# Kernel optimization log

Measured on AMD Instinct MI355X. Metric: run time of the kernel, lower is better.

Reference implementation:

```python
import jax, jax.numpy as jnp
import numpy as np

K = 20
EPS = 1e-5
SLOPE = 0.2


def _knn_idx(x, k):
    # x: [B, C, N] -> idx [B, N, k] of nearest neighbors by squared L2
    sq = jnp.sum(x * x, axis=1)                      # [B, N]
    inner = jnp.einsum('bcn,bcm->bnm', x, x)         # [B, N, N]
    neg_dist = 2.0 * inner - sq[:, :, None] - sq[:, None, :]
    return jax.lax.top_k(neg_dist, k)[1]             # [B, N, k]


def _edge_block(x, W, gamma, beta, k):
    # x: [B, C, N]; W: [O, 2C]; returns [B, O, N]
    idx = _knn_idx(x, k)
    xt = jnp.transpose(x, (0, 2, 1))                 # [B, N, C]
    nb = jax.vmap(lambda t, i: t[i])(xt, idx)        # [B, N, k, C] gather
    ctr = xt[:, :, None, :]
    edge = jnp.concatenate(
        [nb - ctr, jnp.broadcast_to(ctr, nb.shape)], axis=-1)  # [B, N, k, 2C]
    y = jnp.einsum('bnkc,oc->bonk', edge, W)         # 1x1 conv
    # BatchNorm2d (training mode: batch stats over B,N,k per channel)
    m = jnp.mean(y, axis=(0, 2, 3), keepdims=True)
    v = jnp.var(y, axis=(0, 2, 3), keepdims=True)
    y = (y - m) * jax.lax.rsqrt(v + EPS)
    y = y * gamma[None, :, None, None] + beta[None, :, None, None]
    y = jnp.where(y >= 0, y, SLOPE * y)              # LeakyReLU(0.2)
    return jnp.max(y, axis=-1)                       # max over k neighbors


def setup_inputs() -> dict:
    key = jax.random.key(0)
    ks = jax.random.split(key, 8)
    B, N = 8, 2048
    x = jax.random.normal(ks[0], (B, N, 3), dtype=jnp.float32)
    W1 = jax.random.normal(ks[1], (64, 6), dtype=jnp.float32) * 0.2
    W2 = jax.random.normal(ks[2], (128, 128), dtype=jnp.float32) * 0.08
    W3 = jax.random.normal(ks[3], (256, 256), dtype=jnp.float32) * 0.06
    g1, b1 = jnp.ones((64,), jnp.float32), jnp.zeros((64,), jnp.float32)
    g2, b2 = jnp.ones((128,), jnp.float32), jnp.zeros((128,), jnp.float32)
    g3, b3 = jnp.ones((256,), jnp.float32), jnp.zeros((256,), jnp.float32)
    L1 = jax.random.normal(ks[4], (1024, 448), dtype=jnp.float32) * 0.04
    L2 = jax.random.normal(ks[5], (2500, 1024), dtype=jnp.float32) * 0.03
    return {"x": x, "W1": W1, "g1": g1, "b1": b1, "W2": W2, "g2": g2,
            "b2": b2, "W3": W3, "g3": g3, "b3": b3, "L1": L1, "L2": L2}


def reference(x, W1, g1, b1, W2, g2, b2, W3, g3, b3, L1, L2):
    xT = jnp.transpose(x, (0, 2, 1))                 # [B, 3, N]
    x1 = _edge_block(xT, W1, g1, b1, K)              # [B, 64, N]
    x2 = _edge_block(x1, W2, g2, b2, K)              # [B, 128, N]
    x3 = _edge_block(x2, W3, g3, b3, K)              # [B, 256, N]
    feat = jnp.concatenate([x1, x2, x3], axis=1)     # [B, 448, N]
    pooled = jnp.max(feat, axis=-1)                  # adaptive_max_pool1d(1)
    h = pooled @ L1.T
    h = jnp.where(h >= 0, h, SLOPE * h)              # LeakyReLU(0.2)
    # dropout is identity in eval mode
    return h @ L2.T                                  # [B, 2500]
```

## Files before the change

### kernel.cpp

```cpp
#include <hip/hip_runtime.h>
#include <hip/hip_bf16.h>
#include <float.h>

#define K_NN 20
#define EPS 1e-5f
#define SLOPE 0.2f
constexpr int Bsz = 8;
constexpr int Npts = 2048;
constexpr int NQ = 8;
constexpr int BN = Bsz * Npts;

typedef __attribute__((ext_vector_type(8))) short short8v;
typedef __attribute__((ext_vector_type(4))) float f32x4;

__device__ __forceinline__ float dot4(float4 a, float4 b) {
  return a.x*b.x + a.y*b.y + a.z*b.z + a.w*b.w;
}
__device__ __forceinline__ unsigned encf(float f) {
  unsigned u = __float_as_uint(f);
  return (u & 0x80000000u) ? ~u : (u | 0x80000000u);
}
__device__ __forceinline__ float decf(unsigned e) {
  unsigned u = (e & 0x80000000u) ? (e & 0x7fffffffu) : ~e;
  return __uint_as_float(u);
}
__device__ __forceinline__ unsigned short f2bf(float x) {
  unsigned u = __float_as_uint(x);
  unsigned r = (u + 0x7fffu + ((u >> 16) & 1u)) >> 16;
  return (unsigned short)r;
}
__device__ __forceinline__ float bf2f(unsigned short h) {
  return __uint_as_float((unsigned)h << 16);
}
__device__ __forceinline__ f32x4 mfma16(short8v a, short8v b, f32x4 c) {
  return __builtin_amdgcn_mfma_f32_16x16x32_bf16(a, b, c, 0, 0, 0);
}

template<int C>
__global__ __launch_bounds__(256) void sq_kernel(const float* __restrict__ xt,
                                                 float* __restrict__ sq) {
  int p = blockIdx.x * 256 + threadIdx.x;
  if (p >= BN) return;
  const float* r = xt + (size_t)p * C;
  float s = 0.f;
  if constexpr (C % 4 == 0) {
    for (int c4 = 0; c4 < C / 4; ++c4) { float4 v = *(const float4*)(r + c4 * 4); s += dot4(v, v); }
  } else {
    #pragma unroll
    for (int c = 0; c < C; ++c) { float v = r[c]; s += v * v; }
  }
  sq[p] = s;
}

template<int C, int MT>
__global__ __launch_bounds__(256) void knn_part(const float* __restrict__ xt,
    const float* __restrict__ sq, float* __restrict__ pval, int* __restrict__ pidx) {
  constexpr int MQ = Npts / NQ;
  __shared__ __align__(16) float chk[MT][C];
  __shared__ float csq[MT];
  const int t = threadIdx.x, w = t >> 6, l = t & 63;
  const int rowblk = blockIdx.x / NQ;
  const int q = blockIdx.x - rowblk * NQ;
  const int p0 = rowblk * 256;
  const int b = p0 / Npts;
  const int myrow = p0 + w * 64 + l;

  float cr[C];
  #pragma unroll
  for (int c = 0; c < C; ++c) cr[c] = xt[(size_t)myrow * C + c];
  const float sqn = sq[myrow];

  float vals[K_NN]; int ids[K_NN];
  #pragma unroll
  for (int i = 0; i < K_NN; ++i) { vals[i] = -FLT_MAX; ids[i] = 0; }

  const int mbase = q * MQ;
  for (int m0 = mbase; m0 < mbase + MQ; m0 += MT) {
    __syncthreads();
    const float* s2 = xt + ((size_t)b * Npts + m0) * C;
    for (int e = t; e < MT * C; e += 256) chk[e / C][e - (e / C) * C] = s2[e];
    for (int e = t; e < MT; e += 256) csq[e] = sq[b * Npts + m0 + e];
    __syncthreads();
    for (int j = 0; j < MT; ++j) {
      float dt = 0.f;
      #pragma unroll
      for (int c = 0; c < C; ++c) dt += cr[c] * chk[j][c];
      float nd = 2.f * dt - sqn - csq[j];
      if (nd > vals[K_NN - 1]) {
        vals[K_NN - 1] = nd; ids[K_NN - 1] = m0 + j;
        #pragma unroll
        for (int i = K_NN - 1; i >= 1; --i) {
          if (vals[i] > vals[i - 1]) {
            float tv = vals[i]; vals[i] = vals[i-1]; vals[i-1] = tv;
            int ti = ids[i]; ids[i] = ids[i-1]; ids[i-1] = ti;
          }
        }
      }
    }
  }
  size_t base = ((size_t)q * BN + myrow) * K_NN;
  #pragma unroll
  for (int i = 0; i < K_NN; ++i) { pval[base + i] = vals[i]; pidx[base + i] = ids[i]; }
}

__global__ __launch_bounds__(256) void knn_merge(const float* __restrict__ pval,
    const int* __restrict__ pidx, int* __restrict__ idxout) {
  int p = blockIdx.x * 256 + threadIdx.x;
  if (p >= BN) return;
  float vals[K_NN]; int ids[K_NN];
  size_t base = (size_t)p * K_NN;
  #pragma unroll
  for (int i = 0; i < K_NN; ++i) { vals[i] = pval[base + i]; ids[i] = pidx[base + i]; }
  for (int q = 1; q < NQ; ++q) {
    size_t b2 = ((size_t)q * BN + p) * K_NN;
    #pragma unroll
    for (int i = 0; i < K_NN; ++i) {
      float v = pval[b2 + i];
      if (v <= vals[K_NN - 1]) break;
      int m = pidx[b2 + i];
      vals[K_NN - 1] = v; ids[K_NN - 1] = m;
      #pragma unroll
      for (int r = K_NN - 1; r >= 1; --r) {
        if (vals[r] > vals[r - 1]) {
          float tv = vals[r]; vals[r] = vals[r-1]; vals[r-1] = tv;
          int ti = ids[r]; ids[r] = ids[r-1]; ids[r-1] = ti;
        }
      }
    }
  }
  int* op = idxout + (size_t)p * K_NN;
  #pragma unroll
  for (int i = 0; i < K_NN; ++i) op[i] = ids[i];
}

template<int C>
__global__ __launch_bounds__(256, 1) void knn_fused(
    const unsigned short* __restrict__ xh, const unsigned short* __restrict__ xl,
    const float* __restrict__ sq, int* __restrict__ idxout) {
  constexpr int KS = C / 32;
  __shared__ __align__(16) char smem[40960];
  float (*dist)[66] = (float(*)[66])smem;
  float (*lv)[K_NN] = (float(*)[K_NN])smem;
  int   (*li)[K_NN] = (int(*)[K_NN])(smem + 256 * K_NN * 4);
  const int b = blockIdx.x >> 5, nt = blockIdx.x & 31;
  const int n0 = nt * 64;
  const int t = threadIdx.x, l = t & 63, wv = t >> 6, l15 = l & 15, grp = l >> 4;
  const unsigned short* xbh = xh + (size_t)b * Npts * C;
  const unsigned short* xbl = xl + (size_t)b * Npts * C;
  const float* sqb = sq + b * Npts;

  short8v ah[4 * KS], al[4 * KS];
  #pragma unroll
  for (int rt = 0; rt < 4; ++rt)
    #pragma unroll
    for (int ks = 0; ks < KS; ++ks) {
      const size_t a = (size_t)(n0 + rt * 16 + l15) * C + ks * 32 + grp * 8;
      ah[rt * KS + ks] = *(const short8v*)(xbh + a);
      al[rt * KS + ks] = *(const short8v*)(xbl + a);
    }

  const int srow = t >> 2, ss = t & 3;
  const float sqn = sqb[n0 + srow];
  float vals[K_NN]; int ids[K_NN];
  #pragma unroll
  for (int i = 0; i < K_NN; ++i) { vals[i] = -FLT_MAX; ids[i] = 0; }

  for (int mt = 0; mt < 32; ++mt) {
    const int m0 = mt * 64;
    const int brow = m0 + wv * 16 + l15;
    f32x4 acc[4];
    #pragma unroll
    for (int rt = 0; rt < 4; ++rt) acc[rt] = (f32x4){0.f, 0.f, 0.f, 0.f};
    #pragma unroll
    for (int ks = 0; ks < KS; ++ks) {
      const size_t boff = (size_t)brow * C + ks * 32 + grp * 8;
      const short8v bh = *(const short8v*)(xbh + boff);
      const short8v bl = *(const short8v*)(xbl + boff);
      #pragma unroll
      for (int rt = 0; rt < 4; ++rt) {
        acc[rt] = mfma16(ah[rt * KS + ks], bh, acc[rt]);
        acc[rt] = mfma16(al[rt * KS + ks], bh, acc[rt]);
        acc[rt] = mfma16(ah[rt * KS + ks], bl, acc[rt]);
      }
    }
    __syncthreads();
    #pragma unroll
    for (int rt = 0; rt < 4; ++rt)
      #pragma unroll
      for (int r = 0; r < 4; ++r)
        dist[rt * 16 + grp * 4 + r][wv * 16 + l15] = 2.f * acc[rt][r];
    __syncthreads();
    for (int j = 0; j < 16; ++j) {
      const int gcol = m0 + ss * 16 + j;
      float v = dist[srow][ss * 16 + j] - sqn - sqb[gcol];
      if (gcol == n0 + srow) v = 0.f;
      if (v > vals[K_NN - 1]) {
        vals[K_NN - 1] = v; ids[K_NN - 1] = gcol;
        #pragma unroll
        for (int r = K_NN - 1; r >= 1; --r) {
          if (vals[r] > vals[r - 1]) {
            float tv = vals[r]; vals[r] = vals[r-1]; vals[r-1] = tv;
            int ti = ids[r]; ids[r] = ids[r-1]; ids[r-1] = ti;
          }
        }
      }
    }
  }
  __syncthreads();
  #pragma unroll
  for (int i = 0; i < K_NN; ++i) { lv[t][i] = vals[i]; li[t][i] = ids[i]; }
  __syncthreads();
  if (t < 64) {
    float mv[K_NN]; int mi[K_NN];
    #pragma unroll
    for (int i = 0; i < K_NN; ++i) { mv[i] = lv[t * 4][i]; mi[i] = li[t * 4][i]; }
    for (int s2 = 1; s2 < 4; ++s2) {
      #pragma unroll
      for (int i = 0; i < K_NN; ++i) {
        const float v = lv[t * 4 + s2][i];
        if (v <= mv[K_NN - 1]) break;
        const int m = li[t * 4 + s2][i];
        mv[K_NN - 1] = v; mi[K_NN - 1] = m;
        #pragma unroll
        for (int r = K_NN - 1; r >= 1; --r) {
          if (mv[r] > mv[r - 1]) {
            float tv = mv[r]; mv[r] = mv[r-1]; mv[r-1] = tv;
            int ti = mi[r]; mi[r] = mi[r-1]; mi[r-1] = ti;
          }
        }
      }
    }
    int* op = idxout + ((size_t)(b * Npts + n0 + t)) * K_NN;
    #pragma unroll
    for (int i = 0; i < K_NN; ++i) op[i] = mi[i];
  }
}

template<int C, int O>
__global__ __launch_bounds__(256) void prep_w(const float* __restrict__ W,
    unsigned short* __restrict__ wh, unsigned short* __restrict__ wl) {
  int i = blockIdx.x * 256 + threadIdx.x;
  if (i >= 2 * O * C) return;
  int j = i / C, c = i - j * C;
  float v = (j < O) ? W[(size_t)j * 2 * C + c]
                    : (W[(size_t)(j - O) * 2 * C + C + c] - W[(size_t)(j - O) * 2 * C + c]);
  unsigned short h = f2bf(v);
  wh[i] = h; wl[i] = f2bf(v - bf2f(h));
}

template<int C, int N2>
__global__ __launch_bounds__(256) void zgemm(
    const unsigned short* __restrict__ xh, const unsigned short* __restrict__ xl,
    const unsigned short* __restrict__ wh, const unsigned short* __restrict__ wl,
    float* __restrict__ Z, int r0) {
  constexpr int KS = C / 32;
  constexpr int CB = N2 / 64;
  const int nb = blockIdx.x / CB, cb = blockIdx.x - nb * CB;
  const int ln0 = nb * 64;
  const int t = threadIdx.x, l = t & 63, wv = t >> 6, l15 = l & 15, grp = l >> 4;
  const int col = cb * 64 + wv * 16 + l15;
  f32x4 acc[4];
  #pragma unroll
  for (int rt = 0; rt < 4; ++rt) acc[rt] = (f32x4){0.f, 0.f, 0.f, 0.f};
  #pragma unroll
  for (int ks = 0; ks < KS; ++ks) {
    const int krd = ks * 32 + grp * 8;
    const short8v bh = *(const short8v*)(wh + (size_t)col * C + krd);
    const short8v bl = *(const short8v*)(wl + (size_t)col * C + krd);
    #pragma unroll
    for (int rt = 0; rt < 4; ++rt) {
      const size_t arow = (size_t)(r0 + ln0 + rt * 16 + l15) * C + krd;
      const short8v a_h = *(const short8v*)(xh + arow);
      const short8v a_l = *(const short8v*)(xl + arow);
      acc[rt] = mfma16(a_h, bh, acc[rt]);
      acc[rt] = mfma16(a_l, bh, acc[rt]);
      acc[rt] = mfma16(a_h, bl, acc[rt]);
    }
  }
  #pragma unroll
  for (int rt = 0; rt < 4; ++rt)
    #pragma unroll
    for (int r = 0; r < 4; ++r)
      Z[(size_t)(ln0 + rt * 16 + grp * 4 + r) * N2 + col] = acc[rt][r];
}

template<int O, int NPP>
__global__ __launch_bounds__(256) void nbr_reduce(
    const float* __restrict__ Z, const int* __restrict__ idx,
    float* __restrict__ mx, float* __restrict__ mn,
    float* __restrict__ psum, float* __restrict__ psq, int r0) {
  constexpr int PPB = 256 / O;
  constexpr int O2 = 2 * O;
  const int t = threadIdx.x;
  const int o = t % O;
  const int sub = t / O;
  float ls = 0.f, lq = 0.f;
  for (int it = 0; it < NPP / PPB; ++it) {
    const int p = r0 + blockIdx.x * NPP + it * PPB + sub;
    const int bbase = (p >> 11) << 11;
    const int* ip = idx + (size_t)p * K_NN;
    const float base = Z[(size_t)(p - r0) * O2 + O + o];
    float vmx = -FLT_MAX, vmn = FLT_MAX;
    #pragma unroll
    for (int k = 0; k < K_NN; ++k) {
      const int nbrow = bbase + ip[k] - r0;
      const float y = Z[(size_t)nbrow * O2 + o] + base;
      ls += y; lq = fmaf(y, y, lq);
      vmx = fmaxf(vmx, y); vmn = fminf(vmn, y);
    }
    mx[(size_t)p * O + o] = vmx;
    mn[(size_t)p * O + o] = vmn;
  }
  if constexpr (PPB > 1) {
    __shared__ float s1[256], s2[256];
    s1[t] = ls; s2[t] = lq;
    __syncthreads();
    if (sub == 0) {
      psum[(size_t)blockIdx.x * O + o] = ls + s1[t + O];
      psq [(size_t)blockIdx.x * O + o] = lq + s2[t + O];
    }
  } else {
    psum[(size_t)blockIdx.x * O + o] = ls;
    psq [(size_t)blockIdx.x * O + o] = lq;
  }
}

template<int C, int O, int G, int NPG, int CPT>
__global__ __launch_bounds__(256) void edge_kernel(const float* __restrict__ xt,
    const int* __restrict__ idx, const float* __restrict__ W,
    float* __restrict__ mx, float* __restrict__ mn,
    float* __restrict__ psum, float* __restrict__ psq) {
  constexpr int WP = O / (64 * CPT);
  constexpr int TPB = 64 * WP * NPG;
  constexpr int PPG = G / NPG;
  static_assert(TPB == 256, "block must be 256 threads");
  __shared__ __align__(16) float pts[G][K_NN + 1][C];
  __shared__ int ids[G][K_NN + 1];
  __shared__ float shps[NPG][O];
  __shared__ float shpq[NPG][O];
  const int t = threadIdx.x;
  const int p0 = blockIdx.x * G;
  const int b = p0 / Npts;

  for (int e = t; e < G * (K_NN + 1); e += TPB) {
    int g = e / (K_NN + 1), j = e - g * (K_NN + 1);
    ids[g][j] = (j == 0) ? (p0 + g) : (b * Npts + idx[(size_t)(p0 + g) * K_NN + (j - 1)]);
  }
  __syncthreads();
  for (int e = t; e < G * (K_NN + 1) * C; e += TPB) {
    int g = e / ((K_NN + 1) * C), rem = e - g * ((K_NN + 1) * C);
    int j = rem / C, c = rem - j * C;
    pts[g][j][c] = xt[(size_t)ids[g][j] * C + c];
  }
  __syncthreads();

  const int w = t >> 6, l = t & 63;
  const int pg = w / WP, wp = w - pg * WP;
  const int o0 = wp * 64 + l;
  float ls0 = 0.f, lq0 = 0.f;

  for (int it = 0; it < PPG; ++it) {
    const int g = pg * PPG + it;
    float yk0[K_NN];
    float u0 = 0.f, v0 = 0.f;
    #pragma unroll
    for (int k = 0; k < K_NN; ++k) yk0[k] = 0.f;
    const float* W0 = W + (size_t)o0 * (2 * C);
    #pragma unroll
    for (int c = 0; c < C; ++c) {
      const float wl = W0[c], whv = W0[C + c], ccv = pts[g][0][c];
      u0 += wl * ccv; v0 += whv * ccv;
      #pragma unroll
      for (int k = 0; k < K_NN; ++k) yk0[k] += wl * pts[g][k + 1][c];
    }
    const int n = p0 + g - b * Npts;
    const size_t obase = ((size_t)b * Npts + n) * O;
    const float base = v0 - u0;
    float vmx = -FLT_MAX, vmn = FLT_MAX;
    #pragma unroll
    for (int k = 0; k < K_NN; ++k) {
      float y = yk0[k] + base;
      ls0 += y; lq0 += y * y;
      vmx = fmaxf(vmx, y); vmn = fminf(vmn, y);
    }
    mx[obase + o0] = vmx; mn[obase + o0] = vmn;
  }

  shps[pg][o0] = ls0; shpq[pg][o0] = lq0;
  __syncthreads();
  if (t < O) {
    float s = 0.f, qq = 0.f;
    #pragma unroll
    for (int i = 0; i < NPG; ++i) { s += shps[i][t]; qq += shpq[i][t]; }
    psum[(size_t)blockIdx.x * O + t] = s;
    psq [(size_t)blockIdx.x * O + t] = qq;
  }
}

template<int O, int NBLK>
__global__ __launch_bounds__(256) void stats_part(const float* __restrict__ psum,
    const float* __restrict__ psq, double* __restrict__ pp, double* __restrict__ pq) {
  constexpr int NS = 16;
  constexpr int SL = NBLK / NS;
  const int l = threadIdx.x & 63, w = threadIdx.x >> 6;
  const int os = blockIdx.x % (O / 64), sl = blockIdx.x / (O / 64);
  const int o = os * 64 + l;
  double s = 0.0, ss = 0.0;
  for (int i = sl * SL + w; i < (sl + 1) * SL; i += 4) {
    s  += (double)psum[(size_t)i * O + o];
    ss += (double)psq [(size_t)i * O + o];
  }
  __shared__ double sh[2][4][64];
  sh[0][w][l] = s; sh[1][w][l] = ss;
  __syncthreads();
  if (w == 0) {
    s  = sh[0][0][l] + sh[0][1][l] + sh[0][2][l] + sh[0][3][l];
    ss = sh[1][0][l] + sh[1][1][l] + sh[1][2][l] + sh[1][3][l];
    pp[(size_t)sl * O + o] = s;
    pq[(size_t)sl * O + o] = ss;
  }
}

template<int O>
__global__ __launch_bounds__(64) void stats_final(const double* __restrict__ pp,
    const double* __restrict__ pq,
    const float* __restrict__ gamma, const float* __restrict__ beta,
    float* __restrict__ scale, float* __restrict__ bias) {
  const int o = blockIdx.x * 64 + threadIdx.x;
  double s = 0.0, ss = 0.0;
  #pragma unroll
  for (int sl = 0; sl < 16; ++sl) { s += pp[(size_t)sl * O + o]; ss += pq[(size_t)sl * O + o]; }
  double cnt = (double)Bsz * Npts * K_NN;
  double m = s / cnt;
  double var = ss / cnt - m * m;
  float g = gamma[o];
  float sc = g * rsqrtf((float)var + EPS);
  scale[o] = sc;
  bias[o] = beta[o] - (float)m * sc;
}

__global__ __launch_bounds__(256) void reset_pool(unsigned* __restrict__ pooled) {
  int i = blockIdx.x * 256 + threadIdx.x;
  if (i < Bsz * 448) pooled[i] = 0u;
}

template<int O, int COFF, bool WNC>
__global__ __launch_bounds__(256) void apply_kernel(const float* __restrict__ mx,
    const float* __restrict__ mn, const float* __restrict__ scale,
    const float* __restrict__ bias, float* __restrict__ xnc,
    unsigned short* __restrict__ xh, unsigned short* __restrict__ xl,
    unsigned* __restrict__ pooled) {
  constexpr int OT = O / 64;
  constexpr int NCH = Npts / 256;
  const int bid = blockIdx.x;
  const int nchunk = bid % NCH;
  const int ot = (bid / NCH) % OT;
  const int b = bid / (NCH * OT);
  const int l = threadIdx.x & 63, w = threadIdx.x >> 6;
  const int o = ot * 64 + l;
  const float sc = scale[o], bs = bias[o];
  const bool pos = (sc >= 0.f);
  float vmax = -FLT_MAX;
  const int n0 = nchunk * 256;
  for (int i = 0; i < 64; ++i) {
    int n = n0 + w + i * 4;
    size_t ix = ((size_t)b * Npts + n) * O + o;
    float raw = pos ? mx[ix] : mn[ix];
    float y = raw * sc + bs;
    y = (y >= 0.f) ? y : SLOPE * y;
    if constexpr (WNC) {
      xnc[ix] = y;
      unsigned short h = f2bf(y);
      xh[ix] = h;
      xl[ix] = f2bf(y - bf2f(h));
    }
    vmax = fmaxf(vmax, y);
  }
  __shared__ float sh[4][64];
  sh[w][l] = vmax;
  __syncthreads();
  if (w == 0) {
    float m = fmaxf(fmaxf(sh[0][l], sh[1][l]), fmaxf(sh[2][l], sh[3][l]));
    atomicMax(pooled + b * 448 + COFF + o, encf(m));
  }
}

template<int CIN, bool LRELU, bool DECODE>
__global__ __launch_bounds__(64) void fc_kernel(const void* __restrict__ inv,
    const float* __restrict__ Wt, float* __restrict__ out, int JO) {
  int j = blockIdx.x;
  const float* wr = Wt + (size_t)j * CIN;
  float acc[Bsz];
  #pragma unroll
  for (int b = 0; b < Bsz; ++b) acc[b] = 0.f;
  for (int c = threadIdx.x; c < CIN; c += 64) {
    float wv = wr[c];
    #pragma unroll
    for (int b = 0; b < Bsz; ++b) {
      float x;
      if constexpr (DECODE) x = decf(((const unsigned*)inv)[b * CIN + c]);
      else                  x = ((const float*)inv)[b * CIN + c];
      acc[b] += x * wv;
    }
  }
  #pragma unroll
  for (int b = 0; b < Bsz; ++b) {
    float v = acc[b];
    #pragma unroll
    for (int w = 32; w > 0; w >>= 1) v += __shfl_down(v, w);
    if (threadIdx.x == 0) {
      if (LRELU) v = (v >= 0.f) ? v : SLOPE * v;
      out[b * JO + j] = v;
    }
  }
}

extern "C" void kernel_launch(void* const* d_in, const int* in_sizes, int n_in,
                              void* d_out, int out_size, void* d_ws, size_t ws_size,
                              hipStream_t stream) {
  const float* x   = (const float*)d_in[0];
  const float* W1  = (const float*)d_in[1];
  const float* g1  = (const float*)d_in[2];
  const float* b1  = (const float*)d_in[3];
  const float* W2  = (const float*)d_in[4];
  const float* g2  = (const float*)d_in[5];
  const float* b2  = (const float*)d_in[6];
  const float* W3  = (const float*)d_in[7];
  const float* g3  = (const float*)d_in[8];
  const float* b3  = (const float*)d_in[9];
  const float* L1  = (const float*)d_in[10];
  const float* L2  = (const float*)d_in[11];
  float* out = (float*)d_out;

  float* ws = (float*)d_ws;
  size_t off = 0;
  float* sq    = ws + off; off += BN;
  int*   idxb  = (int*)(ws + off); off += (size_t)BN * K_NN;
  float* mx    = ws + off; off += (size_t)BN * 256;
  float* mn    = ws + off; off += (size_t)BN * 256;
  float* Z     = ws + off; off += (size_t)BN * 256;
  float* psum  = ws + off; off += (size_t)2048 * 256;
  float* psq   = ws + off; off += (size_t)2048 * 256;
  off = (off + 1) & ~(size_t)1;
  double* pp   = (double*)(ws + off); off += 16 * 256 * 2;
  double* pq   = (double*)(ws + off); off += 16 * 256 * 2;
  float* scale = ws + off; off += 256;
  float* bias  = ws + off; off += 256;
  float* x1nc  = ws + off; off += (size_t)BN * 64;
  float* x2nc  = ws + off; off += (size_t)BN * 128;
  unsigned short* xh1 = (unsigned short*)(ws + off); off += (size_t)BN * 64 / 2;
  unsigned short* xl1 = (unsigned short*)(ws + off); off += (size_t)BN * 64 / 2;
  unsigned short* xh2 = (unsigned short*)(ws + off); off += (size_t)BN * 128 / 2;
  unsigned short* xl2 = (unsigned short*)(ws + off); off += (size_t)BN * 128 / 2;
  unsigned* pooled = (unsigned*)(ws + off); off += Bsz * 448;
  float* h     = ws + off; off += Bsz * 1024;
  unsigned short* wch2 = (unsigned short*)(ws + off); off += 256 * 64 / 2;
  unsigned short* wcl2 = (unsigned short*)(ws + off); off += 256 * 64 / 2;
  unsigned short* wch3 = (unsigned short*)(ws + off); off += 512 * 128 / 2;
  unsigned short* wcl3 = (unsigned short*)(ws + off); off += 512 * 128 / 2;
  float* pval = mx;
  int*   pidx = (int*)mn;

  reset_pool<<<14, 256, 0, stream>>>(pooled);
  prep_w<64, 128><<<(2 * 128 * 64 + 255) / 256, 256, 0, stream>>>(W2, wch2, wcl2);
  prep_w<128, 256><<<(2 * 256 * 128 + 255) / 256, 256, 0, stream>>>(W3, wch3, wcl3);

  sq_kernel<3><<<64, 256, 0, stream>>>(x, sq);
  knn_part<3, 64><<<(BN / 256) * NQ, 256, 0, stream>>>(x, sq, pval, pidx);
  knn_merge<<<64, 256, 0, stream>>>(pval, pidx, idxb);
  edge_kernel<3, 64, 16, 4, 1><<<BN / 16, 256, 0, stream>>>(x, idxb, W1, mx, mn, psum, psq);
  stats_part<64, 1024><<<16, 256, 0, stream>>>(psum, psq, pp, pq);
  stats_final<64><<<1, 64, 0, stream>>>(pp, pq, g1, b1, scale, bias);
  apply_kernel<64, 0, true><<<64, 256, 0, stream>>>(mx, mn, scale, bias, x1nc, xh1, xl1, pooled);

  sq_kernel<64><<<64, 256, 0, stream>>>(x1nc, sq);
  knn_fused<64><<<Bsz * 32, 256, 0, stream>>>(xh1, xl1, sq, idxb);
  zgemm<64, 256><<<(BN / 64) * 4, 256, 0, stream>>>(xh1, xl1, wch2, wcl2, Z, 0);
  nbr_reduce<128, 16><<<BN / 16, 256, 0, stream>>>(Z, idxb, mx, mn, psum, psq, 0);
  stats_part<128, 1024><<<32, 256, 0, stream>>>(psum, psq, pp, pq);
  stats_final<128><<<2, 64, 0, stream>>>(pp, pq, g2, b2, scale, bias);
  apply_kernel<128, 64, true><<<128, 256, 0, stream>>>(mx, mn, scale, bias, x2nc, xh2, xl2, pooled);

  sq_kernel<128><<<64, 256, 0, stream>>>(x2nc, sq);
  knn_fused<128><<<Bsz * 32, 256, 0, stream>>>(xh2, xl2, sq, idxb);
  for (int pass = 0; pass < 2; ++pass) {
    const int r0 = pass * (BN / 2);
    zgemm<128, 512><<<(BN / 2 / 64) * 8, 256, 0, stream>>>(xh2, xl2, wch3, wcl3, Z, r0);
    nbr_reduce<256, 8><<<BN / 2 / 8, 256, 0, stream>>>(Z, idxb, mx, mn,
        psum + (size_t)pass * 1024 * 256, psq + (size_t)pass * 1024 * 256, r0);
  }
  stats_part<256, 2048><<<64, 256, 0, stream>>>(psum, psq, pp, pq);
  stats_final<256><<<4, 64, 0, stream>>>(pp, pq, g3, b3, scale, bias);
  apply_kernel<256, 192, false><<<256, 256, 0, stream>>>(mx, mn, scale, bias, nullptr, nullptr, nullptr, pooled);

  fc_kernel<448, true, true><<<1024, 64, 0, stream>>>(pooled, L1, h, 1024);
  fc_kernel<1024, false, false><<<2500, 64, 0, stream>>>(h, L2, out, 2500);
}
```

Before: 1.248 ms.

## Restructure knn_fused into single-wave blocks with in-register top-k and shuffle merge

The fused kNN kernel now runs one 64-lane wave per block, each handling 16 query points. Each wave keeps the query fragments in registers and streams all candidate tiles through MFMA. Distances are consumed straight from the accumulator registers, so the LDS staging, the __syncthreads barriers and the LDS-based merge are gone; the four per-lane partial top-k lists are merged with shuffles. This raises block count from 256 to 1024 to fill more CUs. In exchange, the candidate loads are re-read per wave with less reuse across query rows, and the per-lane insertion sorts get more divergent work.

```diff
diff --git a/kernel.cpp b/kernel.cpp
--- a/kernel.cpp
+++ b/kernel.cpp
@@ -134,68 +134,86 @@
 }
 
 template<int C>
-__global__ __launch_bounds__(256, 1) void knn_fused(
+__global__ __launch_bounds__(64) void knn_fused(
     const unsigned short* __restrict__ xh, const unsigned short* __restrict__ xl,
     const float* __restrict__ sq, int* __restrict__ idxout) {
   constexpr int KS = C / 32;
-  __shared__ __align__(16) char smem[40960];
-  float (*dist)[66] = (float(*)[66])smem;
-  float (*lv)[K_NN] = (float(*)[K_NN])smem;
-  int   (*li)[K_NN] = (int(*)[K_NN])(smem + 256 * K_NN * 4);
-  const int b = blockIdx.x >> 5, nt = blockIdx.x & 31;
-  const int n0 = nt * 64;
-  const int t = threadIdx.x, l = t & 63, wv = t >> 6, l15 = l & 15, grp = l >> 4;
+  const int b = blockIdx.x >> 7, qt = blockIdx.x & 127;
+  const int q0 = qt * 16;
+  const int l = threadIdx.x, l15 = l & 15, grp = l >> 4;
   const unsigned short* xbh = xh + (size_t)b * Npts * C;
   const unsigned short* xbl = xl + (size_t)b * Npts * C;
   const float* sqb = sq + b * Npts;
-
-  short8v ah[4 * KS], al[4 * KS];
-  #pragma unroll
-  for (int rt = 0; rt < 4; ++rt)
+  const int qi = q0 + l15;
+
+  short8v bh[KS], bl[KS];
+  #pragma unroll
+  for (int ks = 0; ks < KS; ++ks) {
+    const size_t a = (size_t)qi * C + ks * 32 + grp * 8;
+    bh[ks] = *(const short8v*)(xbh + a);
+    bl[ks] = *(const short8v*)(xbl + a);
+  }
+  const float sqn = sqb[qi];
+
+  float vals[K_NN]; int ids[K_NN];
+  #pragma unroll
+  for (int i = 0; i < K_NN; ++i) { vals[i] = -FLT_MAX; ids[i] = 0; }
+
+  for (int mt = 0; mt < Npts / 64; ++mt) {
+    const int m0 = mt * 64;
+    f32x4 acc[4];
+    #pragma unroll
+    for (int rt = 0; rt < 4; ++rt) acc[rt] = (f32x4){0.f, 0.f, 0.f, 0.f};
     #pragma unroll
     for (int ks = 0; ks < KS; ++ks) {
-      const size_t a = (size_t)(n0 + rt * 16 + l15) * C + ks * 32 + grp * 8;
-      ah[rt * KS + ks] = *(const short8v*)(xbh + a);
-      al[rt * KS + ks] = *(const short8v*)(xbl + a);
-    }
-
-  const int srow = t >> 2, ss = t & 3;
-  const float sqn = sqb[n0 + srow];
-  float vals[K_NN]; int ids[K_NN];
-  #pragma unroll
-  for (int i = 0; i < K_NN; ++i) { vals[i] = -FLT_MAX; ids[i] = 0; }
-
-  for (int mt = 0; mt < 32; ++mt) {
-    const int m0 = mt * 64;
-    const int brow = m0 + wv * 16 + l15;
-    f32x4 acc[4];
-    #pragma unroll
-    for (int rt = 0; rt < 4; ++rt) acc[rt] = (f32x4){0.f, 0.f, 0.f, 0.f};
-    #pragma unroll
-    for (int ks = 0; ks < KS; ++ks) {
-      const size_t boff = (size_t)brow * C + ks * 32 + grp * 8;
-      const short8v bh = *(const short8v*)(xbh + boff);
-      const short8v bl = *(const short8v*)(xbl + boff);
       #pragma unroll
       for (int rt = 0; rt < 4; ++rt) {
-        acc[rt] = mfma16(ah[rt * KS + ks], bh, acc[rt]);
-        acc[rt] = mfma16(al[rt * KS + ks], bh, acc[rt]);
-        acc[rt] = mfma16(ah[rt * KS + ks], bl, acc[rt]);
+        const size_t aoff = (size_t)(m0 + rt * 16 + l15) * C + ks * 32 + grp * 8;
+        const short8v a_h = *(const short8v*)(xbh + aoff);
+        const short8v a_l = *(const short8v*)(xbl + aoff);
+        acc[rt] = mfma16(a_h, bh[ks], acc[rt]);
+        acc[rt] = mfma16(a_l, bh[ks], acc[rt]);
+        acc[rt] = mfma16(a_h, bl[ks], acc[rt]);
       }
     }
-    __syncthreads();
-    #pragma unroll
-    for (int rt = 0; rt < 4; ++rt)
+    #pragma unroll
+    for (int rt = 0; rt < 4; ++rt) {
+      const int cb = m0 + rt * 16 + grp * 4;
+      const float4 s4 = *(const float4*)(sqb + cb);
+      const float sv[4] = {s4.x, s4.y, s4.z, s4.w};
       #pragma unroll
-      for (int r = 0; r < 4; ++r)
-        dist[rt * 16 + grp * 4 + r][wv * 16 + l15] = 2.f * acc[rt][r];
-    __syncthreads();
-    for (int j = 0; j < 16; ++j) {
-      const int gcol = m0 + ss * 16 + j;
-      float v = dist[srow][ss * 16 + j] - sqn - sqb[gcol];
-      if (gcol == n0 + srow) v = 0.f;
-      if (v > vals[K_NN - 1]) {
-        vals[K_NN - 1] = v; ids[K_NN - 1] = gcol;
+      for (int r = 0; r < 4; ++r) {
+        const int cand = cb + r;
+        float v = 2.f * acc[rt][r] - sqn - sv[r];
+        if (cand == qi) v = 0.f;
+        if (v > vals[K_NN - 1]) {
+          vals[K_NN - 1] = v; ids[K_NN - 1] = cand;
+          #pragma unroll
+          for (int i = K_NN - 1; i >= 1; --i) {
+            if (vals[i] > vals[i - 1]) {
+              float tv = vals[i]; vals[i] = vals[i-1]; vals[i-1] = tv;
+              int ti = ids[i]; ids[i] = ids[i-1]; ids[i-1] = ti;
+            }
+          }
+        }
+      }
+    }
+  }
+
+  #pragma unroll
+  for (int s2 = 1; s2 < 4; ++s2) {
+    float ov[K_NN]; int oi[K_NN];
+    #pragma unroll
+    for (int i = 0; i < K_NN; ++i) {
+      ov[i] = __shfl(vals[i], s2 * 16 + l15);
+      oi[i] = __shfl(ids[i],  s2 * 16 + l15);
+    }
+    if (grp == 0) {
+      #pragma unroll
+      for (int i = 0; i < K_NN; ++i) {
+        const float v = ov[i];
+        if (v <= vals[K_NN - 1]) break;
+        vals[K_NN - 1] = v; ids[K_NN - 1] = oi[i];
         #pragma unroll
         for (int r = K_NN - 1; r >= 1; --r) {
           if (vals[r] > vals[r - 1]) {
@@ -206,33 +224,10 @@
       }
     }
   }
-  __syncthreads();
-  #pragma unroll
-  for (int i = 0; i < K_NN; ++i) { lv[t][i] = vals[i]; li[t][i] = ids[i]; }
-  __syncthreads();
-  if (t < 64) {
-    float mv[K_NN]; int mi[K_NN];
-    #pragma unroll
-    for (int i = 0; i < K_NN; ++i) { mv[i] = lv[t * 4][i]; mi[i] = li[t * 4][i]; }
-    for (int s2 = 1; s2 < 4; ++s2) {
-      #pragma unroll
-      for (int i = 0; i < K_NN; ++i) {
-        const float v = lv[t * 4 + s2][i];
-        if (v <= mv[K_NN - 1]) break;
-        const int m = li[t * 4 + s2][i];
-        mv[K_NN - 1] = v; mi[K_NN - 1] = m;
-        #pragma unroll
-        for (int r = K_NN - 1; r >= 1; --r) {
-          if (mv[r] > mv[r - 1]) {
-            float tv = mv[r]; mv[r] = mv[r-1]; mv[r-1] = tv;
-            int ti = mi[r]; mi[r] = mi[r-1]; mi[r-1] = ti;
-          }
-        }
-      }
-    }
-    int* op = idxout + ((size_t)(b * Npts + n0 + t)) * K_NN;
-    #pragma unroll
-    for (int i = 0; i < K_NN; ++i) op[i] = mi[i];
+  if (grp == 0) {
+    int* op = idxout + ((size_t)(b * Npts + qi)) * K_NN;
+    #pragma unroll
+    for (int i = 0; i < K_NN; ++i) op[i] = ids[i];
   }
 }
 
@@ -574,7 +569,7 @@
   apply_kernel<64, 0, true><<<64, 256, 0, stream>>>(mx, mn, scale, bias, x1nc, xh1, xl1, pooled);
 
   sq_kernel<64><<<64, 256, 0, stream>>>(x1nc, sq);
-  knn_fused<64><<<Bsz * 32, 256, 0, stream>>>(xh1, xl1, sq, idxb);
+  knn_fused<64><<<Bsz * 128, 64, 0, stream>>>(xh1, xl1, sq, idxb);
   zgemm<64, 256><<<(BN / 64) * 4, 256, 0, stream>>>(xh1, xl1, wch2, wcl2, Z, 0);
   nbr_reduce<128, 16><<<BN / 16, 256, 0, stream>>>(Z, idxb, mx, mn, psum, psq, 0);
   stats_part<128, 1024><<<32, 256, 0, stream>>>(psum, psq, pp, pq);
@@ -582,7 +577,7 @@
   apply_kernel<128, 64, true><<<128, 256, 0, stream>>>(mx, mn, scale, bias, x2nc, xh2, xl2, pooled);
 
   sq_kernel<128><<<64, 256, 0, stream>>>(x2nc, sq);
-  knn_fused<128><<<Bsz * 32, 256, 0, stream>>>(xh2, xl2, sq, idxb);
+  knn_fused<128><<<Bsz * 128, 64, 0, stream>>>(xh2, xl2, sq, idxb);
   for (int pass = 0; pass < 2; ++pass) {
     const int r0 = pass * (BN / 2);
     zgemm<128, 512><<<(BN / 2 / 64) * 8, 256, 0, stream>>>(xh2, xl2, wch3, wcl3, Z, r0);
```

Result: no change. 1.238 ms (-0.8%).
